# Kernel optimization log

Hardware: AMD Instinct MI355X
Metric: run time of the kernel (lower is better)

## Reference

```python
import math
import jax, jax.numpy as jnp
import numpy as np

NH, NKV, HD = 16, 8, 128  # n_heads, n_kv_heads, head_dim from config

def setup_inputs() -> dict:
    key = jax.random.key(0)
    ks = jax.random.split(key, 5)
    B, T, D = 2, 2048, 2048
    KV = NKV * HD  # 1024
    s = 1.0 / math.sqrt(D)
    return {
        "x": jax.random.normal(ks[0], (B, T, D), dtype=jnp.float32),
        "Wq": jax.random.normal(ks[1], (D, D), dtype=jnp.float32) * s,
        "Wk": jax.random.normal(ks[2], (KV, D), dtype=jnp.float32) * s,
        "Wv": jax.random.normal(ks[3], (KV, D), dtype=jnp.float32) * s,
        "Wo": jax.random.normal(ks[4], (D, D), dtype=jnp.float32) * s,
    }

def reference(x, Wq, Wk, Wv, Wo):
    B, T, D = x.shape
    groups = NH // NKV
    scale = 1.0 / math.sqrt(HD)
    # Projections (torch Linear: y = x @ W.T)
    q = (x @ Wq.T).reshape(B, T, NH, HD).transpose(0, 2, 1, 3)    # [B, nh, T, hd]
    k = (x @ Wk.T).reshape(B, T, NKV, HD).transpose(0, 2, 1, 3)   # [B, nkv, T, hd]
    v = (x @ Wv.T).reshape(B, T, NKV, HD).transpose(0, 2, 1, 3)   # [B, nkv, T, hd]
    kv_state = jnp.concatenate([k, v], axis=-1)                    # [B, nkv, T, 2*hd]
    # GQA: replicate kv heads (repeat_interleave along head dim)
    k = jnp.repeat(k, groups, axis=1)                              # [B, nh, T, hd]
    v = jnp.repeat(v, groups, axis=1)
    scores = jnp.einsum('bhqd,bhkd->bhqk', q, k) * scale           # [B, nh, T, T]
    causal = jnp.tril(jnp.ones((T, T), dtype=bool))
    scores = jnp.where(causal, scores, jnp.finfo(scores.dtype).min)
    probs = jax.nn.softmax(scores, axis=-1)
    attn = jnp.einsum('bhqk,bhkd->bhqd', probs, v)                 # [B, nh, T, hd]
    attn = attn.transpose(0, 2, 1, 3).reshape(B, T, NH * HD)
    output = attn @ Wo.T
    return (output, kv_state)
```

## Files before the change

### kernel.cpp

```cpp
#include <hip/hip_runtime.h>
#include <hip/hip_bf16.h>
#include <cstdint>
#include <cstddef>

#define DEV __device__ __forceinline__

typedef __attribute__((ext_vector_type(8))) short short8;
typedef __attribute__((ext_vector_type(4))) float f32x4;
typedef __attribute__((ext_vector_type(8))) __bf16 bf16x8;

DEV unsigned short f2bf(float f) {
    unsigned u = __builtin_bit_cast(unsigned, f);
    u += 0x7fffu + ((u >> 16) & 1u);
    return (unsigned short)(u >> 16);
}

DEV unsigned short f2bf_hw(float f) {
    return __builtin_bit_cast(unsigned short, (__bf16)f);
}

DEV f32x4 mfma16(short8 a, short8 b, f32x4 c) {
    return __builtin_amdgcn_mfma_f32_16x16x32_bf16(
        __builtin_bit_cast(bf16x8, a), __builtin_bit_cast(bf16x8, b), c, 0, 0, 0);
}

#define GLD_TO_LDS16(g, l)                                                  \
    __builtin_amdgcn_global_load_lds(                                       \
        (const __attribute__((address_space(1))) void*)(g),                 \
        (__attribute__((address_space(3))) void*)(l), 16, 0, 0)

__global__ void cvt_all(const float* __restrict__ x,  const float* __restrict__ wq,
                        const float* __restrict__ wk, const float* __restrict__ wv,
                        const float* __restrict__ wo,
                        unsigned short* __restrict__ xb,  unsigned short* __restrict__ wqb,
                        unsigned short* __restrict__ wkb, unsigned short* __restrict__ wvb,
                        unsigned short* __restrict__ wob) {
    constexpr int NX = 1048576, NQ = 524288, NK = 262144, NV = 262144, NO = 524288;
    constexpr int C1 = NX, C2 = C1 + NQ, C3 = C2 + NK, C4 = C3 + NV, C5 = C4 + NO;
    int i = blockIdx.x * blockDim.x + threadIdx.x;
    int stride = gridDim.x * blockDim.x;
    for (; i < C5; i += stride) {
        const float* s;
        unsigned short* d;
        int j;
        if (i < C1)      { s = x;  d = xb;  j = i; }
        else if (i < C2) { s = wq; d = wqb; j = i - C1; }
        else if (i < C3) { s = wk; d = wkb; j = i - C2; }
        else if (i < C4) { s = wv; d = wvb; j = i - C3; }
        else             { s = wo; d = wob; j = i - C4; }
        const f32x4* sp = (const f32x4*)(s + (size_t)j * 8);
        f32x4 a = sp[0], bq = sp[1];
        short8 o;
        o[0] = (short)f2bf(a[0]);  o[1] = (short)f2bf(a[1]);
        o[2] = (short)f2bf(a[2]);  o[3] = (short)f2bf(a[3]);
        o[4] = (short)f2bf(bq[0]); o[5] = (short)f2bf(bq[1]);
        o[6] = (short)f2bf(bq[2]); o[7] = (short)f2bf(bq[3]);
        *(short8*)(d + (size_t)j * 8) = o;
    }
}

__global__ __launch_bounds__(256) void transpose_v(
    const unsigned short* __restrict__ src, unsigned short* __restrict__ dst) {
    __shared__ __align__(16) unsigned short tile[64 * 64];
    const int t0 = blockIdx.x * 64;
    const int d0 = blockIdx.y * 64;
    const int b  = blockIdx.z;
    const int tid = threadIdx.x;
#pragma unroll
    for (int p = 0; p < 2; ++p) {
        int ch = tid + p * 256;
        int it = ch >> 3, ic8 = ch & 7;
        short8 v = *(const short8*)(src + (size_t)(b * 2048 + t0 + it) * 1024 + d0 + ic8 * 8);
        *(short8*)&tile[it * 64 + ((ic8 ^ (it & 7)) << 3)] = v;
    }
    __syncthreads();
#pragma unroll
    for (int p = 0; p < 2; ++p) {
        int ch = tid + p * 256;
        int od = ch >> 3, ot8 = ch & 7;
        short8 v;
#pragma unroll
        for (int j = 0; j < 8; ++j) {
            int t = ot8 * 8 + j;
            v[j] = (short)tile[t * 64 + ((((od >> 3) ^ (t & 7)) << 3) | (od & 7))];
        }
        *(short8*)(dst + (size_t)(b * 1024 + d0 + od) * 2048 + t0 + ot8 * 8) = v;
    }
}

__global__ __launch_bounds__(512, 2) void gemm_qkv_8p(
    const unsigned short* __restrict__ A,
    const unsigned short* __restrict__ Wq, const unsigned short* __restrict__ Wk,
    const unsigned short* __restrict__ Wv,
    unsigned short* __restrict__ Qo, unsigned short* __restrict__ Ko,
    unsigned short* __restrict__ Vo, float* __restrict__ kvf) {
    constexpr int K = 2048, BM = 256, KT = K / 64;
    __shared__ __align__(16) unsigned short sA[2][2][BM][32];
    __shared__ __align__(16) unsigned short sB[2][2][BM][32];

    const int tid = threadIdx.x, lane = tid & 63, w = tid >> 6;
    const int wm = w >> 2, wn = w & 3;
    const int lrow = lane & 15, lg = lane >> 4;
    const int m0 = blockIdx.y * BM, n0 = blockIdx.x * BM;

    const unsigned short* Bp;
    unsigned short* Co;
    int c0, ostr, doff = 0;
    bool iskv = false;
    if (n0 < 2048)      { Bp = Wq + (size_t)n0 * K;        Co = Qo; c0 = n0;        ostr = 2048; }
    else if (n0 < 3072) { Bp = Wk + (size_t)(n0-2048) * K; Co = Ko; c0 = n0 - 2048; ostr = 1024; iskv = true; }
    else                { Bp = Wv + (size_t)(n0-3072) * K; Co = Vo; c0 = n0 - 3072; ostr = 1024; iskv = true; doff = 128; }

    const unsigned short* Ab = A + (size_t)m0 * K;

    auto stage = [&](const unsigned short* gcol, unsigned short* lds) {
#pragma unroll
        for (int p = 0; p < 2; ++p) {
            int ch = tid + p * 512;
            int row = ch >> 2;
            int slot = (ch & 3) ^ ((row >> 1) & 3);
            GLD_TO_LDS16(gcol + (size_t)row * K + slot * 8, lds + ch * 8);
        }
    };

    f32x4 acc[8][4];
#pragma unroll
    for (int i = 0; i < 8; ++i)
#pragma unroll
        for (int j = 0; j < 4; ++j) acc[i][j] = (f32x4)0.f;

    const int arow0 = wm * 128 + lrow;
    const int brow0 = wn * 64 + lrow;
    auto xr = [&](int row) { return (lg ^ ((row >> 1) & 3)) << 3; };

    stage(Ab,      &sA[0][0][0][0]);
    stage(Bp,      &sB[0][0][0][0]);
    stage(Ab + 32, &sA[0][1][0][0]);
    stage(Bp + 32, &sB[0][1][0][0]);
    asm volatile("s_waitcnt vmcnt(4)\n\ts_barrier" ::: "memory");

    for (int kt = 0; kt < KT; ++kt) {
        const int buf = kt & 1, nb = buf ^ 1;
        const bool pre = (kt + 1 < KT);
        const unsigned short* An = Ab + (kt + 1) * 64;
        const unsigned short* Bn = Bp + (kt + 1) * 64;
        short8 bfrag[4], afrag[4];

        if (pre) stage(An, &sA[nb][0][0][0]);
#pragma unroll
        for (int ni = 0; ni < 4; ++ni)
            bfrag[ni] = *(const short8*)(&sB[buf][0][brow0 + ni * 16][0] + xr(brow0 + ni * 16));
#pragma unroll
        for (int mi = 0; mi < 4; ++mi)
            afrag[mi] = *(const short8*)(&sA[buf][0][arow0 + mi * 16][0] + xr(arow0 + mi * 16));
        __builtin_amdgcn_s_setprio(1);
#pragma unroll
        for (int mi = 0; mi < 4; ++mi)
#pragma unroll
            for (int ni = 0; ni < 4; ++ni)
                acc[mi][ni] = mfma16(afrag[mi], bfrag[ni], acc[mi][ni]);
        __builtin_amdgcn_s_setprio(0);

        if (pre) stage(Bn, &sB[nb][0][0][0]);
#pragma unroll
        for (int mi = 0; mi < 4; ++mi)
            afrag[mi] = *(const short8*)(&sA[buf][0][arow0 + 64 + mi * 16][0] + xr(arow0 + 64 + mi * 16));
        __builtin_amdgcn_s_setprio(1);
#pragma unroll
        for (int mi = 0; mi < 4; ++mi)
#pragma unroll
            for (int ni = 0; ni < 4; ++ni)
                acc[4 + mi][ni] = mfma16(afrag[mi], bfrag[ni], acc[4 + mi][ni]);
        __builtin_amdgcn_s_setprio(0);

        if (pre) asm volatile("s_waitcnt vmcnt(4)\n\ts_barrier" ::: "memory");
        else     asm volatile("s_waitcnt vmcnt(0)\n\ts_barrier" ::: "memory");

        if (pre) stage(An + 32, &sA[nb][1][0][0]);
#pragma unroll
        for (int ni = 0; ni < 4; ++ni)
            bfrag[ni] = *(const short8*)(&sB[buf][1][brow0 + ni * 16][0] + xr(brow0 + ni * 16));
#pragma unroll
        for (int mi = 0; mi < 4; ++mi)
            afrag[mi] = *(const short8*)(&sA[buf][1][arow0 + mi * 16][0] + xr(arow0 + mi * 16));
        __builtin_amdgcn_s_setprio(1);
#pragma unroll
        for (int mi = 0; mi < 4; ++mi)
#pragma unroll
            for (int ni = 0; ni < 4; ++ni)
                acc[mi][ni] = mfma16(afrag[mi], bfrag[ni], acc[mi][ni]);
        __builtin_amdgcn_s_setprio(0);

        if (pre) stage(Bn + 32, &sB[nb][1][0][0]);
#pragma unroll
        for (int mi = 0; mi < 4; ++mi)
            afrag[mi] = *(const short8*)(&sA[buf][1][arow0 + 64 + mi * 16][0] + xr(arow0 + 64 + mi * 16));
        __builtin_amdgcn_s_setprio(1);
#pragma unroll
        for (int mi = 0; mi < 4; ++mi)
#pragma unroll
            for (int ni = 0; ni < 4; ++ni)
                acc[4 + mi][ni] = mfma16(afrag[mi], bfrag[ni], acc[4 + mi][ni]);
        __builtin_amdgcn_s_setprio(0);

        if (pre) asm volatile("s_waitcnt vmcnt(4)\n\ts_barrier" ::: "memory");
    }

    const int lrow4 = (lane >> 4) * 4, lcol = lane & 15;
#pragma unroll
    for (int mi = 0; mi < 8; ++mi) {
#pragma unroll
        for (int ni = 0; ni < 4; ++ni) {
#pragma unroll
            for (int r = 0; r < 4; ++r) {
                int row = m0 + wm * 128 + mi * 16 + lrow4 + r;
                int col = c0 + wn * 64 + ni * 16 + lcol;
                float v = acc[mi][ni][r];
                Co[(size_t)row * ostr + col] = f2bf_hw(v);
                if (iskv) {
                    int b = row >> 11, t = row & 2047;
                    int kh = col >> 7, d = col & 127;
                    kvf[((size_t)(b * 8 + kh) * 2048 + t) * 256 + doff + d] = v;
                }
            }
        }
    }
}

__global__ __launch_bounds__(512, 2) void gemm_o_2p(
    const unsigned short* __restrict__ A, const unsigned short* __restrict__ Bm,
    float* __restrict__ Cf) {
    constexpr int K = 2048, N = 2048, KT = K / 64;
    __shared__ __align__(16) unsigned short sA[2][2][256][32];
    __shared__ __align__(16) unsigned short sB[2][2][128][32];

    const int tid = threadIdx.x, lane = tid & 63, w = tid >> 6;
    const int wm = w >> 1, wn = w & 1;
    const int lrow = lane & 15, lg = lane >> 4;
    const int m0 = blockIdx.y * 256, n0 = blockIdx.x * 128;

    const unsigned short* Ab = A + (size_t)m0 * K;
    const unsigned short* Bb = Bm + (size_t)n0 * K;

    auto stageA = [&](const unsigned short* gcol, unsigned short* lds) {
#pragma unroll
        for (int p = 0; p < 2; ++p) {
            int ch = tid + p * 512;
            int row = ch >> 2;
            int slot = (ch & 3) ^ ((row >> 1) & 3);
            GLD_TO_LDS16(gcol + (size_t)row * K + slot * 8, lds + ch * 8);
        }
    };
    auto stageB = [&](const unsigned short* gcol, unsigned short* lds) {
        int ch = tid;
        int row = ch >> 2;
        int slot = (ch & 3) ^ ((row >> 1) & 3);
        GLD_TO_LDS16(gcol + (size_t)row * K + slot * 8, lds + ch * 8);
    };

    f32x4 acc[4][4];
#pragma unroll
    for (int i = 0; i < 4; ++i)
#pragma unroll
        for (int j = 0; j < 4; ++j) acc[i][j] = (f32x4)0.f;

    const int arow0 = wm * 64 + lrow;
    const int brow0 = wn * 64 + lrow;
    auto xr = [&](int row) { return (lg ^ ((row >> 1) & 3)) << 3; };

    stageA(Ab,      &sA[0][0][0][0]);
    stageB(Bb,      &sB[0][0][0][0]);
    stageA(Ab + 32, &sA[0][1][0][0]);
    stageB(Bb + 32, &sB[0][1][0][0]);
    asm volatile("s_waitcnt vmcnt(3)\n\ts_barrier" ::: "memory");

    for (int kt = 0; kt < KT; ++kt) {
        const int buf = kt & 1, nb = buf ^ 1;
        const bool pre = (kt + 1 < KT);
        const unsigned short* An = Ab + (kt + 1) * 64;
        const unsigned short* Bn = Bb + (kt + 1) * 64;
        short8 afrag[4], bfrag[4];

        if (pre) { stageA(An, &sA[nb][0][0][0]); stageB(Bn, &sB[nb][0][0][0]); }
#pragma unroll
        for (int ni = 0; ni < 4; ++ni)
            bfrag[ni] = *(const short8*)(&sB[buf][0][brow0 + ni * 16][0] + xr(brow0 + ni * 16));
#pragma unroll
        for (int mi = 0; mi < 4; ++mi)
            afrag[mi] = *(const short8*)(&sA[buf][0][arow0 + mi * 16][0] + xr(arow0 + mi * 16));
        __builtin_amdgcn_s_setprio(1);
#pragma unroll
        for (int mi = 0; mi < 4; ++mi)
#pragma unroll
            for (int ni = 0; ni < 4; ++ni)
                acc[mi][ni] = mfma16(afrag[mi], bfrag[ni], acc[mi][ni]);
        __builtin_amdgcn_s_setprio(0);

        if (pre) asm volatile("s_waitcnt vmcnt(3)\n\ts_barrier" ::: "memory");
        else     asm volatile("s_waitcnt vmcnt(0)\n\ts_barrier" ::: "memory");

        if (pre) { stageA(An + 32, &sA[nb][1][0][0]); stageB(Bn + 32, &sB[nb][1][0][0]); }
#pragma unroll
        for (int ni = 0; ni < 4; ++ni)
            bfrag[ni] = *(const short8*)(&sB[buf][1][brow0 + ni * 16][0] + xr(brow0 + ni * 16));
#pragma unroll
        for (int mi = 0; mi < 4; ++mi)
            afrag[mi] = *(const short8*)(&sA[buf][1][arow0 + mi * 16][0] + xr(arow0 + mi * 16));
        __builtin_amdgcn_s_setprio(1);
#pragma unroll
        for (int mi = 0; mi < 4; ++mi)
#pragma unroll
            for (int ni = 0; ni < 4; ++ni)
                acc[mi][ni] = mfma16(afrag[mi], bfrag[ni], acc[mi][ni]);
        __builtin_amdgcn_s_setprio(0);

        if (pre) asm volatile("s_waitcnt vmcnt(3)\n\ts_barrier" ::: "memory");
    }

    const int lrow4 = (lane >> 4) * 4, lcol = lane & 15;
#pragma unroll
    for (int mi = 0; mi < 4; ++mi)
#pragma unroll
        for (int ni = 0; ni < 4; ++ni)
#pragma unroll
            for (int r = 0; r < 4; ++r) {
                int row = m0 + wm * 64 + mi * 16 + lrow4 + r;
                int col = n0 + wn * 64 + ni * 16 + lcol;
                Cf[(size_t)row * N + col] = acc[mi][ni][r];
            }
}

__global__ __launch_bounds__(512, 4) void attn_fwd(
    const unsigned short* __restrict__ Qb, const unsigned short* __restrict__ Kb,
    const unsigned short* __restrict__ Vtg, unsigned short* __restrict__ Ob) {
    constexpr int T = 2048, DQ = 2048, DKV = 1024, HD = 128;
    constexpr float SC2 = 0.08838834764831845f * 1.4426950408889634f;
    constexpr float SHIFT = 8.0f * 1.4426950408889634f;
    __shared__ __align__(16) unsigned short Ks[64 * 136];
    __shared__ __align__(16) unsigned short Vs[128 * 72];
    __shared__ __align__(16) unsigned short Ps[8][16 * 72];

    const int bx = blockIdx.x, kh = blockIdx.y, b = blockIdx.z;
    const int qtile = b ? (31 - bx) : bx;
    const int tid = threadIdx.x, lane = tid & 63, w = tid >> 6;
    const int h = kh * 2 + (w >> 2);
    const int lrow = lane & 15, lg = lane >> 4;
    const int qt0 = qtile * 64;
    const int qrow0 = qt0 + (w & 3) * 16;
    const size_t bT = (size_t)b * T;

    short8 qf[4];
    {
        const unsigned short* qbase = Qb + (bT + qrow0 + lrow) * DQ + h * HD + lg * 8;
#pragma unroll
        for (int kc = 0; kc < 4; ++kc) qf[kc] = *(const short8*)(qbase + kc * 32);
    }

    int kr[2], kc8[2], vd[2], vk8[2];
#pragma unroll
    for (int p = 0; p < 2; ++p) {
        int ch = tid + p * 512;
        kr[p] = ch >> 4;  kc8[p] = ch & 15;
        vd[p] = ch >> 3;  vk8[p] = ch & 7;
    }
    const unsigned short* kbase = Kb + bT * DKV + kh * HD;
    const unsigned short* vbase = Vtg + (size_t)(b * 8 + kh) * 128 * T;
    short8 kreg[2], vreg[2];
    auto gload = [&](int kt) {
#pragma unroll
        for (int p = 0; p < 2; ++p) {
            kreg[p] = *(const short8*)(kbase + (size_t)(kt * 64 + kr[p]) * DKV + kc8[p] * 8);
            vreg[p] = *(const short8*)(vbase + (size_t)vd[p] * T + kt * 64 + vk8[p] * 8);
        }
    };
    auto lwrite = [&]() {
#pragma unroll
        for (int p = 0; p < 2; ++p) {
            *(short8*)&Ks[kr[p] * 136 + kc8[p] * 8] = kreg[p];
            *(short8*)&Vs[vd[p] * 72 + vk8[p] * 8] = vreg[p];
        }
    };

    f32x4 o[8];
#pragma unroll
    for (int i = 0; i < 8; ++i) o[i] = (f32x4)0.f;
    float rsum[4] = {0.f, 0.f, 0.f, 0.f};

    const int nkt = qtile + 1;
    gload(0);
    for (int kt = 0; kt < nkt; ++kt) {
        const int kt0 = kt * 64;
        __syncthreads();
        lwrite();
        __syncthreads();
        if (kt + 1 < nkt) gload(kt + 1);

        f32x4 s[4];
        __builtin_amdgcn_s_setprio(1);
#pragma unroll
        for (int nt = 0; nt < 4; ++nt) {
            s[nt] = (f32x4)0.f;
#pragma unroll
            for (int kc = 0; kc < 4; ++kc) {
                short8 kf = *(const short8*)&Ks[(nt * 16 + lrow) * 136 + kc * 32 + lg * 8];
                s[nt] = mfma16(qf[kc], kf, s[nt]);
            }
        }
        __builtin_amdgcn_s_setprio(0);

        const int qabs = qrow0 + lg * 4;
        const bool diag = (kt == qtile);
#pragma unroll
        for (int nt = 0; nt < 4; ++nt) {
            int kcol = kt0 + nt * 16 + lrow;
#pragma unroll
            for (int r = 0; r < 4; ++r) {
                float p = exp2f(fmaf(s[nt][r], SC2, -SHIFT));
                if (diag && kcol > qabs + r) p = 0.f;
                rsum[r] += p;
                Ps[w][(lg * 4 + r) * 72 + nt * 16 + lrow] = f2bf_hw(p);
            }
        }

        __builtin_amdgcn_s_setprio(1);
#pragma unroll
        for (int kc2 = 0; kc2 < 2; ++kc2) {
            short8 pf = *(const short8*)&Ps[w][lrow * 72 + kc2 * 32 + lg * 8];
#pragma unroll
            for (int dt = 0; dt < 8; ++dt) {
                short8 vf = *(const short8*)&Vs[(dt * 16 + lrow) * 72 + kc2 * 32 + lg * 8];
                o[dt] = mfma16(pf, vf, o[dt]);
            }
        }
        __builtin_amdgcn_s_setprio(0);
    }

#pragma unroll
    for (int r = 0; r < 4; ++r) {
        float v = rsum[r];
        v += __shfl_xor(v, 1);
        v += __shfl_xor(v, 2);
        v += __shfl_xor(v, 4);
        v += __shfl_xor(v, 8);
        float inv = 1.f / v;
        int row = qrow0 + lg * 4 + r;
        unsigned short* obase = Ob + (bT + row) * DQ + h * HD + lrow;
#pragma unroll
        for (int dt = 0; dt < 8; ++dt) obase[dt * 16] = f2bf_hw(o[dt][r] * inv);
    }
}

extern "C" void kernel_launch(void* const* d_in, const int* in_sizes, int n_in,
                              void* d_out, int out_size, void* d_ws, size_t ws_size,
                              hipStream_t stream) {
    (void)in_sizes; (void)n_in; (void)out_size; (void)ws_size;
    const float* x  = (const float*)d_in[0];
    const float* Wq = (const float*)d_in[1];
    const float* Wk = (const float*)d_in[2];
    const float* Wv = (const float*)d_in[3];
    const float* Wo = (const float*)d_in[4];
    float* out = (float*)d_out;
    float* kv_out = out + (size_t)8388608;

    unsigned short* xb   = (unsigned short*)d_ws;
    unsigned short* wqb  = xb   + 8388608;
    unsigned short* wkb  = wqb  + 4194304;
    unsigned short* wvb  = wkb  + 2097152;
    unsigned short* wob  = wvb  + 2097152;
    unsigned short* qb   = wob  + 4194304;
    unsigned short* kb   = qb   + 8388608;
    unsigned short* vt   = kb   + 4194304;
    unsigned short* ab   = vt   + 4194304;
    unsigned short* vtmp = ab;

    cvt_all<<<dim3(2048), dim3(256), 0, stream>>>(x, Wq, Wk, Wv, Wo,
                                                  xb, wqb, wkb, wvb, wob);
    gemm_qkv_8p<<<dim3(16, 16), 512, 0, stream>>>(xb, wqb, wkb, wvb, qb, kb, vtmp, kv_out);
    transpose_v<<<dim3(32, 16, 2), 256, 0, stream>>>(vtmp, vt);
    attn_fwd<<<dim3(32, 8, 2), 512, 0, stream>>>(qb, kb, vt, ab);
    gemm_o_2p<<<dim3(16, 16), 512, 0, stream>>>(ab, wob, out);
}
```

Measured before the change: 237.5 us.

## Fuse V transpose into QKV GEMM epilogue and use direct-to-LDS loads in attention

The QKV GEMM epilogue now writes V already transposed into the Vt buffer using 4-wide packed stores, so the separate transpose_v kernel and its launch go away. The attention kernel now stages K and V tiles with global-to-LDS loads into XOR-swizzled, unpadded shared layouts instead of loading through registers. It processes P in two 32-wide halves with a smaller P buffer, and raises the occupancy hint to 6 blocks. In exchange, the register-based prefetch of the next K/V tile is dropped and each iteration waits with vmcnt(0) before computing, which exposes load latency. The transposed V stores from the GEMM are also strided.

```diff
diff --git a/kernel.cpp b/kernel.cpp
--- a/kernel.cpp
+++ b/kernel.cpp
@@ -6,6 +6,7 @@
 #define DEV __device__ __forceinline__
 
 typedef __attribute__((ext_vector_type(8))) short short8;
+typedef __attribute__((ext_vector_type(4))) short short4v;
 typedef __attribute__((ext_vector_type(4))) float f32x4;
 typedef __attribute__((ext_vector_type(8))) __bf16 bf16x8;
 
@@ -59,41 +60,12 @@
     }
 }
 
-__global__ __launch_bounds__(256) void transpose_v(
-    const unsigned short* __restrict__ src, unsigned short* __restrict__ dst) {
-    __shared__ __align__(16) unsigned short tile[64 * 64];
-    const int t0 = blockIdx.x * 64;
-    const int d0 = blockIdx.y * 64;
-    const int b  = blockIdx.z;
-    const int tid = threadIdx.x;
-#pragma unroll
-    for (int p = 0; p < 2; ++p) {
-        int ch = tid + p * 256;
-        int it = ch >> 3, ic8 = ch & 7;
-        short8 v = *(const short8*)(src + (size_t)(b * 2048 + t0 + it) * 1024 + d0 + ic8 * 8);
-        *(short8*)&tile[it * 64 + ((ic8 ^ (it & 7)) << 3)] = v;
-    }
-    __syncthreads();
-#pragma unroll
-    for (int p = 0; p < 2; ++p) {
-        int ch = tid + p * 256;
-        int od = ch >> 3, ot8 = ch & 7;
-        short8 v;
-#pragma unroll
-        for (int j = 0; j < 8; ++j) {
-            int t = ot8 * 8 + j;
-            v[j] = (short)tile[t * 64 + ((((od >> 3) ^ (t & 7)) << 3) | (od & 7))];
-        }
-        *(short8*)(dst + (size_t)(b * 1024 + d0 + od) * 2048 + t0 + ot8 * 8) = v;
-    }
-}
-
 __global__ __launch_bounds__(512, 2) void gemm_qkv_8p(
     const unsigned short* __restrict__ A,
     const unsigned short* __restrict__ Wq, const unsigned short* __restrict__ Wk,
     const unsigned short* __restrict__ Wv,
     unsigned short* __restrict__ Qo, unsigned short* __restrict__ Ko,
-    unsigned short* __restrict__ Vo, float* __restrict__ kvf) {
+    unsigned short* __restrict__ Vt, float* __restrict__ kvf) {
     constexpr int K = 2048, BM = 256, KT = K / 64;
     __shared__ __align__(16) unsigned short sA[2][2][BM][32];
     __shared__ __align__(16) unsigned short sB[2][2][BM][32];
@@ -104,12 +76,11 @@
     const int m0 = blockIdx.y * BM, n0 = blockIdx.x * BM;
 
     const unsigned short* Bp;
-    unsigned short* Co;
-    int c0, ostr, doff = 0;
-    bool iskv = false;
-    if (n0 < 2048)      { Bp = Wq + (size_t)n0 * K;        Co = Qo; c0 = n0;        ostr = 2048; }
-    else if (n0 < 3072) { Bp = Wk + (size_t)(n0-2048) * K; Co = Ko; c0 = n0 - 2048; ostr = 1024; iskv = true; }
-    else                { Bp = Wv + (size_t)(n0-3072) * K; Co = Vo; c0 = n0 - 3072; ostr = 1024; iskv = true; doff = 128; }
+    unsigned short* Co = nullptr;
+    int c0, mode;
+    if (n0 < 2048)      { Bp = Wq + (size_t)n0 * K;        Co = Qo; c0 = n0;        mode = 0; }
+    else if (n0 < 3072) { Bp = Wk + (size_t)(n0-2048) * K; Co = Ko; c0 = n0 - 2048; mode = 1; }
+    else                { Bp = Wv + (size_t)(n0-3072) * K;           c0 = n0 - 3072; mode = 2; }
 
     const unsigned short* Ab = A + (size_t)m0 * K;
 
@@ -211,16 +182,31 @@
     for (int mi = 0; mi < 8; ++mi) {
 #pragma unroll
         for (int ni = 0; ni < 4; ++ni) {
-#pragma unroll
-            for (int r = 0; r < 4; ++r) {
-                int row = m0 + wm * 128 + mi * 16 + lrow4 + r;
-                int col = c0 + wn * 64 + ni * 16 + lcol;
-                float v = acc[mi][ni][r];
-                Co[(size_t)row * ostr + col] = f2bf_hw(v);
-                if (iskv) {
-                    int b = row >> 11, t = row & 2047;
-                    int kh = col >> 7, d = col & 127;
-                    kvf[((size_t)(b * 8 + kh) * 2048 + t) * 256 + doff + d] = v;
+            int colb = c0 + wn * 64 + ni * 16 + lcol;
+            int row0 = m0 + wm * 128 + mi * 16 + lrow4;
+            if (mode == 2) {
+                int b = row0 >> 11, t = row0 & 2047;
+                int kh = colb >> 7, d = colb & 127;
+                short4v pk;
+#pragma unroll
+                for (int r = 0; r < 4; ++r) {
+                    float v = acc[mi][ni][r];
+                    pk[r] = (short)f2bf_hw(v);
+                    kvf[((size_t)(b * 8 + kh) * 2048 + t + r) * 256 + 128 + d] = v;
+                }
+                *(short4v*)&Vt[((size_t)(b * 1024) + colb) * 2048 + t] = pk;
+            } else {
+                const int ostr = (mode == 0) ? 2048 : 1024;
+#pragma unroll
+                for (int r = 0; r < 4; ++r) {
+                    int row = row0 + r;
+                    float v = acc[mi][ni][r];
+                    Co[(size_t)row * ostr + colb] = f2bf_hw(v);
+                    if (mode == 1) {
+                        int b = row >> 11, t = row & 2047;
+                        int kh = colb >> 7, d = colb & 127;
+                        kvf[((size_t)(b * 8 + kh) * 2048 + t) * 256 + d] = v;
+                    }
                 }
             }
         }
@@ -330,15 +316,15 @@
             }
 }
 
-__global__ __launch_bounds__(512, 4) void attn_fwd(
+__global__ __launch_bounds__(512, 6) void attn_fwd(
     const unsigned short* __restrict__ Qb, const unsigned short* __restrict__ Kb,
     const unsigned short* __restrict__ Vtg, unsigned short* __restrict__ Ob) {
     constexpr int T = 2048, DQ = 2048, DKV = 1024, HD = 128;
     constexpr float SC2 = 0.08838834764831845f * 1.4426950408889634f;
     constexpr float SHIFT = 8.0f * 1.4426950408889634f;
-    __shared__ __align__(16) unsigned short Ks[64 * 136];
-    __shared__ __align__(16) unsigned short Vs[128 * 72];
-    __shared__ __align__(16) unsigned short Ps[8][16 * 72];
+    __shared__ __align__(16) unsigned short Ks[64 * 128];
+    __shared__ __align__(16) unsigned short Vs[128 * 64];
+    __shared__ __align__(16) unsigned short Ps[8][16 * 40];
 
     const int bx = blockIdx.x, kh = blockIdx.y, b = blockIdx.z;
     const int qtile = b ? (31 - bx) : bx;
@@ -356,28 +342,21 @@
         for (int kc = 0; kc < 4; ++kc) qf[kc] = *(const short8*)(qbase + kc * 32);
     }
 
-    int kr[2], kc8[2], vd[2], vk8[2];
-#pragma unroll
-    for (int p = 0; p < 2; ++p) {
-        int ch = tid + p * 512;
-        kr[p] = ch >> 4;  kc8[p] = ch & 15;
-        vd[p] = ch >> 3;  vk8[p] = ch & 7;
-    }
     const unsigned short* kbase = Kb + bT * DKV + kh * HD;
     const unsigned short* vbase = Vtg + (size_t)(b * 8 + kh) * 128 * T;
-    short8 kreg[2], vreg[2];
-    auto gload = [&](int kt) {
+
+    auto stage = [&](int kt) {
 #pragma unroll
         for (int p = 0; p < 2; ++p) {
-            kreg[p] = *(const short8*)(kbase + (size_t)(kt * 64 + kr[p]) * DKV + kc8[p] * 8);
-            vreg[p] = *(const short8*)(vbase + (size_t)vd[p] * T + kt * 64 + vk8[p] * 8);
-        }
-    };
-    auto lwrite = [&]() {
+            int ch = tid + p * 512;
+            int kr = ch >> 4, g = (ch & 15) ^ (kr & 15);
+            GLD_TO_LDS16(kbase + (size_t)(kt * 64 + kr) * DKV + g * 8, Ks + ch * 8);
+        }
 #pragma unroll
         for (int p = 0; p < 2; ++p) {
-            *(short8*)&Ks[kr[p] * 136 + kc8[p] * 8] = kreg[p];
-            *(short8*)&Vs[vd[p] * 72 + vk8[p] * 8] = vreg[p];
+            int ch = tid + p * 512;
+            int d = ch >> 3, g = (ch & 7) ^ (d & 7);
+            GLD_TO_LDS16(vbase + (size_t)d * T + kt * 64 + g * 8, Vs + ch * 8);
         }
     };
 
@@ -387,13 +366,12 @@
     float rsum[4] = {0.f, 0.f, 0.f, 0.f};
 
     const int nkt = qtile + 1;
-    gload(0);
     for (int kt = 0; kt < nkt; ++kt) {
         const int kt0 = kt * 64;
         __syncthreads();
-        lwrite();
+        stage(kt);
+        asm volatile("s_waitcnt vmcnt(0)" ::: "memory");
         __syncthreads();
-        if (kt + 1 < nkt) gload(kt + 1);
 
         f32x4 s[4];
         __builtin_amdgcn_s_setprio(1);
@@ -402,7 +380,7 @@
             s[nt] = (f32x4)0.f;
 #pragma unroll
             for (int kc = 0; kc < 4; ++kc) {
-                short8 kf = *(const short8*)&Ks[(nt * 16 + lrow) * 136 + kc * 32 + lg * 8];
+                short8 kf = *(const short8*)&Ks[(nt * 16 + lrow) * 128 + (((kc * 4 + lg) ^ lrow) << 3)];
                 s[nt] = mfma16(qf[kc], kf, s[nt]);
             }
         }
@@ -411,28 +389,29 @@
         const int qabs = qrow0 + lg * 4;
         const bool diag = (kt == qtile);
 #pragma unroll
-        for (int nt = 0; nt < 4; ++nt) {
-            int kcol = kt0 + nt * 16 + lrow;
-#pragma unroll
-            for (int r = 0; r < 4; ++r) {
-                float p = exp2f(fmaf(s[nt][r], SC2, -SHIFT));
-                if (diag && kcol > qabs + r) p = 0.f;
-                rsum[r] += p;
-                Ps[w][(lg * 4 + r) * 72 + nt * 16 + lrow] = f2bf_hw(p);
+        for (int h2 = 0; h2 < 2; ++h2) {
+#pragma unroll
+            for (int nt2 = 0; nt2 < 2; ++nt2) {
+                int nt = h2 * 2 + nt2;
+                int kcol = kt0 + nt * 16 + lrow;
+#pragma unroll
+                for (int r = 0; r < 4; ++r) {
+                    float p = exp2f(fmaf(s[nt][r], SC2, -SHIFT));
+                    if (diag && kcol > qabs + r) p = 0.f;
+                    rsum[r] += p;
+                    Ps[w][(lg * 4 + r) * 40 + nt2 * 16 + lrow] = f2bf_hw(p);
+                }
             }
-        }
-
-        __builtin_amdgcn_s_setprio(1);
-#pragma unroll
-        for (int kc2 = 0; kc2 < 2; ++kc2) {
-            short8 pf = *(const short8*)&Ps[w][lrow * 72 + kc2 * 32 + lg * 8];
+            short8 pf = *(const short8*)&Ps[w][lrow * 40 + lg * 8];
+            __builtin_amdgcn_s_setprio(1);
 #pragma unroll
             for (int dt = 0; dt < 8; ++dt) {
-                short8 vf = *(const short8*)&Vs[(dt * 16 + lrow) * 72 + kc2 * 32 + lg * 8];
+                int d = dt * 16 + lrow;
+                short8 vf = *(const short8*)&Vs[d * 64 + (((h2 * 4 + lg) ^ (d & 7)) << 3)];
                 o[dt] = mfma16(pf, vf, o[dt]);
             }
-        }
-        __builtin_amdgcn_s_setprio(0);
+            __builtin_amdgcn_s_setprio(0);
+        }
     }
 
 #pragma unroll
@@ -471,12 +450,10 @@
     unsigned short* kb   = qb   + 8388608;
     unsigned short* vt   = kb   + 4194304;
     unsigned short* ab   = vt   + 4194304;
-    unsigned short* vtmp = ab;
 
     cvt_all<<<dim3(2048), dim3(256), 0, stream>>>(x, Wq, Wk, Wv, Wo,
                                                   xb, wqb, wkb, wvb, wob);
-    gemm_qkv_8p<<<dim3(16, 16), 512, 0, stream>>>(xb, wqb, wkb, wvb, qb, kb, vtmp, kv_out);
-    transpose_v<<<dim3(32, 16, 2), 256, 0, stream>>>(vtmp, vt);
+    gemm_qkv_8p<<<dim3(16, 16), 512, 0, stream>>>(xb, wqb, wkb, wvb, qb, kb, vt, kv_out);
     attn_fwd<<<dim3(32, 8, 2), 512, 0, stream>>>(qb, kb, vt, ab);
     gemm_o_2p<<<dim3(16, 16), 512, 0, stream>>>(ab, wob, out);
 }
```

New measurement: 326.7 us. 1.38x slower.
